# Kernel tuning notes

Hardware: AMD Instinct MI355X
Metric: run time of the kernel (lower is better)

## Reference

```python
import jax, jax.numpy as jnp
import numpy as np

B, N, D = 512, 128, 768
TAU = 1.0            # NeuralSort temperature (allRank default)
COS_W = 0.1          # cosine_loss_weight
EPS = 1e-10          # allRank DEFAULT_EPS
PAD = -1.0           # allRank PADDED_Y_VALUE
SINKHORN_ITERS = 50
SINKHORN_TOL = 1e-6


def setup_inputs() -> dict:
    key = jax.random.key(0)
    kq, kr, ky = jax.random.split(key, 3)
    return {
        "query_embeddings": jax.random.normal(kq, (B, N, D), jnp.float32),
        "response_embeddings": jax.random.normal(kr, (B, N, D), jnp.float32),
        "labels": jax.random.uniform(ky, (B, N), dtype=jnp.float32),
    }


def _cosine_similarity(a, b):
    # torch.cosine_similarity semantics: clamp each norm at 1e-8
    num = jnp.sum(a * b, axis=-1)
    den = jnp.maximum(jnp.linalg.norm(a, axis=-1), 1e-8) * jnp.maximum(jnp.linalg.norm(b, axis=-1), 1e-8)
    return num / den


def _deterministic_neural_sort(s, tau, mask):
    # s: [B, N, 1] scores; mask: [B, N] padding mask (True = padded)
    n = s.shape[1]
    s = jnp.where(mask[:, :, None], -1e8, s)
    A = jnp.abs(s - jnp.swapaxes(s, 1, 2))                       # [B,N,N]
    pair_or = mask[:, :, None] | mask[:, None, :]
    A = jnp.where(pair_or, 0.0, A)
    Bmat = jnp.sum(A, axis=2, keepdims=True)                     # == A @ (1 1^T), broadcasts over cols
    valid = n - jnp.sum(mask, axis=1)                            # [B] number of non-padded items
    idx = jnp.arange(n)
    # per-row scaling vector: (n-m) - 1 - 2*j for j < n-m, else 0
    scaling = jnp.where(idx[None, :] < valid[:, None],
                        (valid[:, None] - 1 - 2 * idx[None, :]).astype(s.dtype), 0.0)
    s0 = jnp.where(mask[:, :, None], 0.0, s)
    C = s0 * scaling[:, None, :]                                 # [B,N,N] = s @ scaling^T
    P_max = jnp.swapaxes(C - Bmat, 1, 2)
    P_max = jnp.where(pair_or, -jnp.inf, P_max)
    P_max = jnp.where(mask[:, :, None] & mask[:, None, :], 1.0, P_max)
    return jax.nn.softmax(P_max / tau, axis=-1)


def _sinkhorn(mat, mask):
    pair_or = mask[:, None, :] | mask[:, :, None]
    pair_and = mask[:, None, :] & mask[:, :, None]
    mat = jnp.where(pair_or, 0.0, mat)
    mat = jnp.where(pair_and, 1.0, mat)

    def step(carry, _):
        m, done = carry
        m1 = m / jnp.maximum(jnp.sum(m, axis=1, keepdims=True), EPS)
        m2 = m1 / jnp.maximum(jnp.sum(m1, axis=2, keepdims=True), EPS)
        conv = (jnp.max(jnp.abs(jnp.sum(m2, axis=2) - 1.0)) < SINKHORN_TOL) & \
               (jnp.max(jnp.abs(jnp.sum(m2, axis=1) - 1.0)) < SINKHORN_TOL)
        new_m = jnp.where(done, m, m2)   # freeze once converged (emulates torch early break)
        return (new_m, done | conv), None

    (mat, _), _ = jax.lax.scan(step, (mat, jnp.array(False)), None, length=SINKHORN_ITERS)
    mat = jnp.where(pair_or, 0.0, mat)
    mat = jnp.where(pair_and, 1.0, mat)
    return mat


def _idcg_at_k(y_true, k):
    # allRank dcg(y_true, y_true, ats=[k]) with powered gains (no padding present)
    sorted_true = -jnp.sort(-y_true, axis=1)                     # descending
    gains = jnp.power(2.0, sorted_true) - 1.0
    discounts = 1.0 / jnp.log2(jnp.arange(y_true.shape[1], dtype=jnp.float32) + 2.0)
    return jnp.cumsum(gains * discounts, axis=1)[:, k - 1]       # [B]


def _forward(query_embeddings, response_embeddings, labels):
    scores = _cosine_similarity(query_embeddings, response_embeddings)   # [B,N]
    y_true = labels
    mask = (y_true == PAD)
    k = N                                                                # k=None -> slate length
    P_hat = _deterministic_neural_sort(scores[:, :, None], TAU, mask)    # [B,N,N]
    P_hat = _sinkhorn(P_hat, mask)
    P_hat = jnp.where(mask[:, :, None] | mask[:, None, :], 0.0, P_hat)
    g = jnp.power(2.0, jnp.where(mask, 0.0, y_true)) - 1.0               # powered relevancies
    ground_truth = jnp.einsum('bij,bj->bi', P_hat, g)                    # approx-sorted gains
    discounts = 1.0 / jnp.log2(jnp.arange(N, dtype=jnp.float32) + 2.0)
    discounted = ground_truth * discounts
    idcg = _idcg_at_k(y_true, k)                                         # [B]
    ndcg = jnp.sum(discounted[:, :k], axis=-1) / (idcg + EPS)
    idcg_zero = idcg == 0.0
    ndcg = jnp.where(idcg_zero, 0.0, ndcg)
    mean_ndcg = jnp.sum(ndcg) / jnp.maximum(jnp.sum(~idcg_zero), 1)
    ndcg_loss = 1.0 - mean_ndcg                                          # 1 + neuralNDCG = 1 - mean_ndcg
    cosine_loss = jnp.mean((scores - labels) ** 2)
    return (1.0 - COS_W) * ndcg_loss + COS_W * cosine_loss


def reference(query_embeddings, response_embeddings, labels):
    return _forward(query_embeddings, response_embeddings, labels)
```

## Files before the change

kernel.cpp:

```cpp
#include <hip/hip_runtime.h>
#include <math.h>

#define BB 512
#define NN 128
#define DD 768
#define SSTR 132
#define S4 (SSTR/4)

__global__ __launch_bounds__(256) void k_scores(const float* __restrict__ q,
                                                const float* __restrict__ r,
                                                float* __restrict__ scores) {
    const int tid  = threadIdx.x;
    const int lane = tid & 63;
    const int row  = blockIdx.x * 4 + (tid >> 6);
    const float4* q4 = (const float4*)(q + (size_t)row * DD);
    const float4* r4 = (const float4*)(r + (size_t)row * DD);
    float qr = 0.f, qq = 0.f, rr = 0.f;
#pragma unroll
    for (int k = 0; k < 3; ++k) {
        float4 a = q4[lane + 64 * k];
        float4 b = r4[lane + 64 * k];
        qr += a.x*b.x + a.y*b.y + a.z*b.z + a.w*b.w;
        qq += a.x*a.x + a.y*a.y + a.z*a.z + a.w*a.w;
        rr += b.x*b.x + b.y*b.y + b.z*b.z + b.w*b.w;
    }
#pragma unroll
    for (int off = 32; off >= 1; off >>= 1) {
        qr += __shfl_xor(qr, off);
        qq += __shfl_xor(qq, off);
        rr += __shfl_xor(rr, off);
    }
    if (lane == 0) {
        float den = fmaxf(sqrtf(qq), 1e-8f) * fmaxf(sqrtf(rr), 1e-8f);
        scores[row] = qr / den;
    }
}

__global__ __launch_bounds__(256, 2) void k_ndcg(const float* __restrict__ scores,
                                                 const float* __restrict__ labels,
                                                 float* __restrict__ ndcg_out,
                                                 float* __restrict__ valid_out) {
    extern __shared__ float sm[];
    float* M      = sm;
    float* s_s    = sm + NN * SSTR;
    float* s_B    = s_s + NN;
    float* s_cs   = s_B + NN;
    float* s_rc   = s_cs + NN;
    float* s_g    = s_rc + NN;
    float* s_lab  = s_g + NN;
    float* s_red  = s_lab + NN;
    float* s_misc = s_red + NN;

    const int tid = threadIdx.x;
    const int b   = blockIdx.x;
    const int i   = tid >> 1;
    const int h   = tid & 1;
    const int cc  = tid >> 3;
    const int gg  = tid & 7;
    float4* M4 = (float4*)M;
    const float4* rc4 = (const float4*)s_rc;
    const float4* g4  = (const float4*)s_g;
    const float4* s4a = (const float4*)s_s;
    const float4* B4a = (const float4*)s_B;

    if (tid < NN) {
        float sv = scores[b * NN + tid];
        float lv = labels[b * NN + tid];
        s_s[tid]   = sv;
        s_lab[tid] = lv;
        s_g[tid]   = exp2f(lv) - 1.0f;
    }
    __syncthreads();

    if (tid < NN) {
        float si = s_s[tid];
        float acc = 0.f;
        for (int j = 0; j < NN; ++j) acc += fabsf(si - s_s[j]);
        s_B[tid] = acc;
        float li = s_lab[tid];
        int rank = 0;
        for (int j = 0; j < NN; ++j) {
            float lj = s_lab[j];
            rank += (lj > li) || (lj == li && j < tid);
        }
        s_red[tid] = s_g[tid] / log2f((float)(rank + 2));
    }
    __syncthreads();
    if (tid < 32) {
        float v = s_red[tid] + s_red[tid + 32] + s_red[tid + 64] + s_red[tid + 96];
#pragma unroll
        for (int off = 16; off >= 1; off >>= 1) v += __shfl_xor(v, off);
        if (tid == 0) s_misc[1] = v;
    }

    {
        const float scal = (float)(127 - 2 * i);
        float4 w[16];
        float rmax = -1e30f;
#pragma unroll
        for (int k = 0; k < 16; ++k) {
            float4 sv = s4a[16 * h + k];
            float4 Bv = B4a[16 * h + k];
            float4 v;
            v.x = sv.x * scal - Bv.x;
            v.y = sv.y * scal - Bv.y;
            v.z = sv.z * scal - Bv.z;
            v.w = sv.w * scal - Bv.w;
            w[k] = v;
            rmax = fmaxf(rmax, fmaxf(fmaxf(v.x, v.y), fmaxf(v.z, v.w)));
        }
        rmax = fmaxf(rmax, __shfl_xor(rmax, 1));
        float rsum = 0.f;
#pragma unroll
        for (int k = 0; k < 16; ++k) {
            float4 v = w[k];
            v.x = expf(v.x - rmax);
            v.y = expf(v.y - rmax);
            v.z = expf(v.z - rmax);
            v.w = expf(v.w - rmax);
            w[k] = v;
            rsum += v.x + v.y + v.z + v.w;
        }
        rsum += __shfl_xor(rsum, 1);
        float inv = 1.0f / rsum;
#pragma unroll
        for (int k = 0; k < 16; ++k) {
            float4 v = w[k];
            v.x *= inv; v.y *= inv; v.z *= inv; v.w *= inv;
            M4[i * S4 + 16 * h + k] = v;
        }
    }
    __syncthreads();

    for (int it = 0; it < 50; ++it) {
        float4 acc; acc.x = acc.y = acc.z = acc.w = 0.f;
#pragma unroll
        for (int k = 0; k < 16; ++k) {
            float4 v = M4[(gg * 16 + k) * S4 + cc];
            acc.x += v.x; acc.y += v.y; acc.z += v.z; acc.w += v.w;
        }
#pragma unroll
        for (int off = 4; off >= 1; off >>= 1) {
            acc.x += __shfl_xor(acc.x, off);
            acc.y += __shfl_xor(acc.y, off);
            acc.z += __shfl_xor(acc.z, off);
            acc.w += __shfl_xor(acc.w, off);
        }
        if (gg == 0) ((float4*)s_cs)[cc] = acc;
        __syncthreads();
        if (tid < NN) {
            float c = s_cs[tid];
            s_rc[tid]  = 1.0f / fmaxf(c, 1e-10f);
            s_red[tid] = fabsf(c - 1.0f);
        }
        __syncthreads();
        if (tid < 32) {
            float m = fmaxf(fmaxf(s_red[tid], s_red[tid + 32]),
                            fmaxf(s_red[tid + 64], s_red[tid + 96]));
#pragma unroll
            for (int off = 16; off >= 1; off >>= 1) m = fmaxf(m, __shfl_xor(m, off));
            if (tid == 0) s_misc[0] = m;
        }
        __syncthreads();
        if (it > 0 && s_misc[0] < 1e-6f) break;

        float4 w[16];
        float acc2 = 0.f;
#pragma unroll
        for (int k = 0; k < 16; ++k) {
            float4 v  = M4[i * S4 + 16 * h + k];
            float4 rv = rc4[16 * h + k];
            v.x *= rv.x; v.y *= rv.y; v.z *= rv.z; v.w *= rv.w;
            w[k] = v;
            acc2 += v.x + v.y + v.z + v.w;
        }
        acc2 += __shfl_xor(acc2, 1);
        float rrv = 1.0f / fmaxf(acc2, 1e-10f);
#pragma unroll
        for (int k = 0; k < 16; ++k) {
            float4 v = w[k];
            v.x *= rrv; v.y *= rrv; v.z *= rrv; v.w *= rrv;
            M4[i * S4 + 16 * h + k] = v;
        }
        __syncthreads();
    }

    {
        float acc = 0.f;
#pragma unroll
        for (int k = 0; k < 16; ++k) {
            float4 v  = M4[i * S4 + 16 * h + k];
            float4 gv = g4[16 * h + k];
            acc += v.x * gv.x + v.y * gv.y + v.z * gv.z + v.w * gv.w;
        }
        acc += __shfl_xor(acc, 1);
        if (h == 0) s_red[i] = acc / log2f((float)(i + 2));
    }
    __syncthreads();
    if (tid < 32) {
        float v = s_red[tid] + s_red[tid + 32] + s_red[tid + 64] + s_red[tid + 96];
#pragma unroll
        for (int off = 16; off >= 1; off >>= 1) v += __shfl_xor(v, off);
        if (tid == 0) {
            float idcg = s_misc[1];
            bool zero = (idcg == 0.0f);
            ndcg_out[b]  = zero ? 0.0f : v / (idcg + 1e-10f);
            valid_out[b] = zero ? 0.0f : 1.0f;
        }
    }
}

__global__ __launch_bounds__(256) void k_final(const float* __restrict__ scores,
                                               const float* __restrict__ labels,
                                               const float* __restrict__ ndcg,
                                               const float* __restrict__ valid,
                                               float* __restrict__ out) {
    __shared__ float red[3][4];
    const int tid = threadIdx.x;
    const int lane = tid & 63, wv = tid >> 6;
    float nsum = ndcg[tid] + ndcg[tid + 256];
    float vsum = valid[tid] + valid[tid + 256];
    float csum = 0.f;
    const float4* s4 = (const float4*)scores;
    const float4* l4 = (const float4*)labels;
    for (int idx = tid; idx < (BB * NN / 4); idx += 256) {
        float4 sv = s4[idx], lv = l4[idx];
        float dx = sv.x - lv.x, dy = sv.y - lv.y, dz = sv.z - lv.z, dw = sv.w - lv.w;
        csum += dx * dx + dy * dy + dz * dz + dw * dw;
    }
#pragma unroll
    for (int off = 32; off >= 1; off >>= 1) {
        nsum += __shfl_xor(nsum, off);
        vsum += __shfl_xor(vsum, off);
        csum += __shfl_xor(csum, off);
    }
    if (lane == 0) { red[0][wv] = nsum; red[1][wv] = vsum; red[2][wv] = csum; }
    __syncthreads();
    if (tid == 0) {
        float n = red[0][0] + red[0][1] + red[0][2] + red[0][3];
        float v = red[1][0] + red[1][1] + red[1][2] + red[1][3];
        float c = red[2][0] + red[2][1] + red[2][2] + red[2][3];
        float mean_ndcg = n / fmaxf(v, 1.0f);
        float loss = 0.9f * (1.0f - mean_ndcg) + 0.1f * (c / (float)(BB * NN));
        out[0] = loss;
    }
}

extern "C" void kernel_launch(void* const* d_in, const int* in_sizes, int n_in,
                              void* d_out, int out_size, void* d_ws, size_t ws_size,
                              hipStream_t stream) {
    const float* q   = (const float*)d_in[0];
    const float* r   = (const float*)d_in[1];
    const float* lab = (const float*)d_in[2];
    float* scores = (float*)d_ws;
    float* ndcg   = scores + BB * NN;
    float* valid  = ndcg + BB;
    float* out    = (float*)d_out;

    k_scores<<<BB * NN / 4, 256, 0, stream>>>(q, r, scores);

    const size_t smem = (size_t)(NN * SSTR + 7 * NN + 16) * sizeof(float);
    hipFuncSetAttribute((const void*)k_ndcg,
                        hipFuncAttributeMaxDynamicSharedMemorySize, (int)smem);
    k_ndcg<<<BB, 256, smem, stream>>>(scores, lab, ndcg, valid);

    k_final<<<1, 256, 0, stream>>>(scores, lab, ndcg, valid, out);
}
```

Measured before the change: 528.7 us.

## Fuse cosine-score computation and MSE partials into the per-batch NDCG kernel

Drops the separate scores kernel: each NDCG block now computes its own 128 cosine scores straight from the query and response embeddings and writes them into shared memory. The per-batch MSE partial is also computed inside the block, so the final kernel no longer re-reads scores and labels. The Sinkhorn column-sum mapping is changed so the cross-lane reduction happens within a wavefront, and the row-scale and convergence-check stages are merged to save a barrier per iteration. In exchange, the 512 blocks (capped at 2 per CU by launch bounds) must stream all of q and r, which may use bandwidth less well than the earlier wide grid of 16384 blocks.

Measured after the change: 498.7 us. 5.7% less time.

```diff
diff --git a/kernel.cpp b/kernel.cpp
--- a/kernel.cpp
+++ b/kernel.cpp
@@ -7,39 +7,12 @@
 #define SSTR 132
 #define S4 (SSTR/4)
 
-__global__ __launch_bounds__(256) void k_scores(const float* __restrict__ q,
-                                                const float* __restrict__ r,
-                                                float* __restrict__ scores) {
-    const int tid  = threadIdx.x;
-    const int lane = tid & 63;
-    const int row  = blockIdx.x * 4 + (tid >> 6);
-    const float4* q4 = (const float4*)(q + (size_t)row * DD);
-    const float4* r4 = (const float4*)(r + (size_t)row * DD);
-    float qr = 0.f, qq = 0.f, rr = 0.f;
-#pragma unroll
-    for (int k = 0; k < 3; ++k) {
-        float4 a = q4[lane + 64 * k];
-        float4 b = r4[lane + 64 * k];
-        qr += a.x*b.x + a.y*b.y + a.z*b.z + a.w*b.w;
-        qq += a.x*a.x + a.y*a.y + a.z*a.z + a.w*a.w;
-        rr += b.x*b.x + b.y*b.y + b.z*b.z + b.w*b.w;
-    }
-#pragma unroll
-    for (int off = 32; off >= 1; off >>= 1) {
-        qr += __shfl_xor(qr, off);
-        qq += __shfl_xor(qq, off);
-        rr += __shfl_xor(rr, off);
-    }
-    if (lane == 0) {
-        float den = fmaxf(sqrtf(qq), 1e-8f) * fmaxf(sqrtf(rr), 1e-8f);
-        scores[row] = qr / den;
-    }
-}
-
-__global__ __launch_bounds__(256, 2) void k_ndcg(const float* __restrict__ scores,
+__global__ __launch_bounds__(256, 2) void k_ndcg(const float* __restrict__ q,
+                                                 const float* __restrict__ r,
                                                  const float* __restrict__ labels,
                                                  float* __restrict__ ndcg_out,
-                                                 float* __restrict__ valid_out) {
+                                                 float* __restrict__ valid_out,
+                                                 float* __restrict__ mse_out) {
     extern __shared__ float sm[];
     float* M      = sm;
     float* s_s    = sm + NN * SSTR;
@@ -49,14 +22,15 @@
     float* s_g    = s_rc + NN;
     float* s_lab  = s_g + NN;
     float* s_red  = s_lab + NN;
-    float* s_misc = s_red + NN;
+    float* s_mse  = s_red + NN;
+    float* s_misc = s_mse + NN;
 
     const int tid = threadIdx.x;
     const int b   = blockIdx.x;
+    const int wv  = tid >> 6;
+    const int ln  = tid & 63;
     const int i   = tid >> 1;
     const int h   = tid & 1;
-    const int cc  = tid >> 3;
-    const int gg  = tid & 7;
     float4* M4 = (float4*)M;
     const float4* rc4 = (const float4*)s_rc;
     const float4* g4  = (const float4*)s_g;
@@ -64,11 +38,36 @@
     const float4* B4a = (const float4*)s_B;
 
     if (tid < NN) {
-        float sv = scores[b * NN + tid];
         float lv = labels[b * NN + tid];
-        s_s[tid]   = sv;
         s_lab[tid] = lv;
         s_g[tid]   = exp2f(lv) - 1.0f;
+    }
+
+    const float4* q4 = (const float4*)(q + (size_t)b * NN * DD);
+    const float4* r4 = (const float4*)(r + (size_t)b * NN * DD);
+    for (int m = 0; m < 32; ++m) {
+        const int row = wv + 4 * m;
+        const float4* qa = q4 + row * (DD / 4);
+        const float4* ra = r4 + row * (DD / 4);
+        float qr = 0.f, qq = 0.f, rr2 = 0.f;
+#pragma unroll
+        for (int k = 0; k < 3; ++k) {
+            float4 a = qa[ln + 64 * k];
+            float4 c = ra[ln + 64 * k];
+            qr  += a.x*c.x + a.y*c.y + a.z*c.z + a.w*c.w;
+            qq  += a.x*a.x + a.y*a.y + a.z*a.z + a.w*a.w;
+            rr2 += c.x*c.x + c.y*c.y + c.z*c.z + c.w*c.w;
+        }
+#pragma unroll
+        for (int off = 32; off >= 1; off >>= 1) {
+            qr  += __shfl_xor(qr, off);
+            qq  += __shfl_xor(qq, off);
+            rr2 += __shfl_xor(rr2, off);
+        }
+        if (ln == 0) {
+            float den = fmaxf(sqrtf(qq), 1e-8f) * fmaxf(sqrtf(rr2), 1e-8f);
+            s_s[row] = qr / den;
+        }
     }
     __syncthreads();
 
@@ -84,6 +83,8 @@
             rank += (lj > li) || (lj == li && j < tid);
         }
         s_red[tid] = s_g[tid] / log2f((float)(rank + 2));
+        float d = si - li;
+        s_mse[tid] = d * d;
     }
     __syncthreads();
     if (tid < 32) {
@@ -91,6 +92,12 @@
 #pragma unroll
         for (int off = 16; off >= 1; off >>= 1) v += __shfl_xor(v, off);
         if (tid == 0) s_misc[1] = v;
+    } else if (tid < 64) {
+        int t2 = tid - 32;
+        float v = s_mse[t2] + s_mse[t2 + 32] + s_mse[t2 + 64] + s_mse[t2 + 96];
+#pragma unroll
+        for (int off = 16; off >= 1; off >>= 1) v = v + __shfl_xor(v, off);
+        if (t2 == 0) mse_out[b] = v;
     }
 
     {
@@ -132,34 +139,32 @@
     }
     __syncthreads();
 
+    const int gg2 = ln >> 3;
+    const int cc  = (wv << 3) | (ln & 7);
     for (int it = 0; it < 50; ++it) {
         float4 acc; acc.x = acc.y = acc.z = acc.w = 0.f;
 #pragma unroll
         for (int k = 0; k < 16; ++k) {
-            float4 v = M4[(gg * 16 + k) * S4 + cc];
+            float4 v = M4[(gg2 * 16 + k) * S4 + cc];
             acc.x += v.x; acc.y += v.y; acc.z += v.z; acc.w += v.w;
         }
 #pragma unroll
-        for (int off = 4; off >= 1; off >>= 1) {
+        for (int off = 32; off >= 8; off >>= 1) {
             acc.x += __shfl_xor(acc.x, off);
             acc.y += __shfl_xor(acc.y, off);
             acc.z += __shfl_xor(acc.z, off);
             acc.w += __shfl_xor(acc.w, off);
         }
-        if (gg == 0) ((float4*)s_cs)[cc] = acc;
+        if (gg2 == 0) ((float4*)s_cs)[cc] = acc;
         __syncthreads();
-        if (tid < NN) {
-            float c = s_cs[tid];
-            s_rc[tid]  = 1.0f / fmaxf(c, 1e-10f);
-            s_red[tid] = fabsf(c - 1.0f);
-        }
-        __syncthreads();
-        if (tid < 32) {
-            float m = fmaxf(fmaxf(s_red[tid], s_red[tid + 32]),
-                            fmaxf(s_red[tid + 64], s_red[tid + 96]));
-#pragma unroll
-            for (int off = 16; off >= 1; off >>= 1) m = fmaxf(m, __shfl_xor(m, off));
-            if (tid == 0) s_misc[0] = m;
+        if (tid < 64) {
+            float c0 = s_cs[tid], c1 = s_cs[tid + 64];
+            s_rc[tid]      = 1.0f / fmaxf(c0, 1e-10f);
+            s_rc[tid + 64] = 1.0f / fmaxf(c1, 1e-10f);
+            float dev = fmaxf(fabsf(c0 - 1.0f), fabsf(c1 - 1.0f));
+#pragma unroll
+            for (int off = 32; off >= 1; off >>= 1) dev = fmaxf(dev, __shfl_xor(dev, off));
+            if (tid == 0) s_misc[0] = dev;
         }
         __syncthreads();
         if (it > 0 && s_misc[0] < 1e-6f) break;
@@ -210,39 +215,30 @@
     }
 }
 
-__global__ __launch_bounds__(256) void k_final(const float* __restrict__ scores,
-                                               const float* __restrict__ labels,
-                                               const float* __restrict__ ndcg,
+__global__ __launch_bounds__(256) void k_final(const float* __restrict__ ndcg,
                                                const float* __restrict__ valid,
+                                               const float* __restrict__ mse,
                                                float* __restrict__ out) {
     __shared__ float red[3][4];
     const int tid = threadIdx.x;
     const int lane = tid & 63, wv = tid >> 6;
     float nsum = ndcg[tid] + ndcg[tid + 256];
     float vsum = valid[tid] + valid[tid + 256];
-    float csum = 0.f;
-    const float4* s4 = (const float4*)scores;
-    const float4* l4 = (const float4*)labels;
-    for (int idx = tid; idx < (BB * NN / 4); idx += 256) {
-        float4 sv = s4[idx], lv = l4[idx];
-        float dx = sv.x - lv.x, dy = sv.y - lv.y, dz = sv.z - lv.z, dw = sv.w - lv.w;
-        csum += dx * dx + dy * dy + dz * dz + dw * dw;
-    }
+    float msum = mse[tid] + mse[tid + 256];
 #pragma unroll
     for (int off = 32; off >= 1; off >>= 1) {
         nsum += __shfl_xor(nsum, off);
         vsum += __shfl_xor(vsum, off);
-        csum += __shfl_xor(csum, off);
-    }
-    if (lane == 0) { red[0][wv] = nsum; red[1][wv] = vsum; red[2][wv] = csum; }
+        msum += __shfl_xor(msum, off);
+    }
+    if (lane == 0) { red[0][wv] = nsum; red[1][wv] = vsum; red[2][wv] = msum; }
     __syncthreads();
     if (tid == 0) {
         float n = red[0][0] + red[0][1] + red[0][2] + red[0][3];
         float v = red[1][0] + red[1][1] + red[1][2] + red[1][3];
-        float c = red[2][0] + red[2][1] + red[2][2] + red[2][3];
+        float m = red[2][0] + red[2][1] + red[2][2] + red[2][3];
         float mean_ndcg = n / fmaxf(v, 1.0f);
-        float loss = 0.9f * (1.0f - mean_ndcg) + 0.1f * (c / (float)(BB * NN));
-        out[0] = loss;
+        out[0] = 0.9f * (1.0f - mean_ndcg) + 0.1f * (m / (float)(BB * NN));
     }
 }
 
@@ -252,17 +248,15 @@
     const float* q   = (const float*)d_in[0];
     const float* r   = (const float*)d_in[1];
     const float* lab = (const float*)d_in[2];
-    float* scores = (float*)d_ws;
-    float* ndcg   = scores + BB * NN;
-    float* valid  = ndcg + BB;
-    float* out    = (float*)d_out;
-
-    k_scores<<<BB * NN / 4, 256, 0, stream>>>(q, r, scores);
-
-    const size_t smem = (size_t)(NN * SSTR + 7 * NN + 16) * sizeof(float);
+    float* ndcg  = (float*)d_ws;
+    float* valid = ndcg + BB;
+    float* mse   = valid + BB;
+    float* out   = (float*)d_out;
+
+    const size_t smem = (size_t)(NN * SSTR + 8 * NN + 16) * sizeof(float);
     hipFuncSetAttribute((const void*)k_ndcg,
                         hipFuncAttributeMaxDynamicSharedMemorySize, (int)smem);
-    k_ndcg<<<BB, 256, smem, stream>>>(scores, lab, ndcg, valid);
-
-    k_final<<<1, 256, 0, stream>>>(scores, lab, ndcg, valid, out);
+    k_ndcg<<<BB, 256, smem, stream>>>(q, r, lab, ndcg, valid, mse);
+
+    k_final<<<1, 256, 0, stream>>>(ndcg, valid, mse, out);
 }
```
